# Kernel tuning notes

Hardware: AMD Instinct MI355X
Metric: run time of the kernel (lower is better)

Reference implementation:

```python
import jax, jax.numpy as jnp
import numpy as np

N_NODES = 100000
N_EDGES = 1600000
IN_CH = 128
HID_CH = 128


def setup_inputs() -> dict:
    key = jax.random.key(0)
    ks = jax.random.split(key, 12)
    s = 1.0 / np.sqrt(IN_CH)
    sh = 1.0 / np.sqrt(HID_CH)
    return {
        "x": jax.random.normal(ks[0], (N_NODES, IN_CH), dtype=jnp.float32),
        "edge_index": jax.random.randint(ks[1], (2, N_EDGES), 0, N_NODES, dtype=jnp.int32),
        # SAGEConv1: lin_l (applied to aggregated neighbors, has bias), lin_r (root)
        "W1_l": jax.random.uniform(ks[2], (IN_CH, HID_CH), jnp.float32, -s, s),
        "b1": jax.random.uniform(ks[3], (HID_CH,), jnp.float32, -s, s),
        "W1_r": jax.random.uniform(ks[4], (IN_CH, HID_CH), jnp.float32, -s, s),
        # SAGEConv2
        "W2_l": jax.random.uniform(ks[5], (HID_CH, HID_CH), jnp.float32, -sh, sh),
        "b2": jax.random.uniform(ks[6], (HID_CH,), jnp.float32, -sh, sh),
        "W2_r": jax.random.uniform(ks[7], (HID_CH, HID_CH), jnp.float32, -sh, sh),
        # decoder Linear(hidden, in)
        "Wd": jax.random.uniform(ks[8], (HID_CH, IN_CH), jnp.float32, -sh, sh),
        "bd": jax.random.uniform(ks[9], (IN_CH,), jnp.float32, -sh, sh),
        "alpha": jnp.float32(0.5),
    }


def _sage_conv(h, src, dst, n_nodes, W_l, b, W_r):
    # PyG SAGEConv (mean aggr): out = lin_l(mean_{j in N(i)} x_j) + lin_r(x_i)
    msg = h[src]  # [E, C] gather from source nodes
    agg = jax.ops.segment_sum(msg, dst, num_segments=n_nodes)  # [N, C]
    cnt = jax.ops.segment_sum(jnp.ones((src.shape[0],), h.dtype), dst,
                              num_segments=n_nodes)  # [N]
    mean = agg / jnp.maximum(cnt, 1.0)[:, None]
    return mean @ W_l + b + h @ W_r


def reference(x, edge_index, W1_l, b1, W1_r, W2_l, b2, W2_r, Wd, bd, alpha):
    n_nodes = x.shape[0]
    src, dst = edge_index[0], edge_index[1]
    h = jax.nn.relu(_sage_conv(x, src, dst, n_nodes, W1_l, b1, W1_r))
    # dropout p=0.2 is identity in eval mode
    h = jax.nn.relu(_sage_conv(h, src, dst, n_nodes, W2_l, b2, W2_r))
    x_updated = h @ Wd + bd
    return alpha * x_updated + (1.0 - alpha) * x
```

## Files before the change

### kernel.cpp

```cpp
#include <hip/hip_runtime.h>
#include <cstddef>
#include <cstdint>

#define CH 128
#define NBKT 196
#define ABLK 320
#define BKT_NODES 512

typedef __attribute__((ext_vector_type(8))) short short8;
typedef __attribute__((ext_vector_type(4))) float f32x4;

__device__ __forceinline__ unsigned short f2bf(float f) {
  unsigned u = __float_as_uint(f);
  u += 0x7FFF + ((u >> 16) & 1);
  return (unsigned short)(u >> 16);
}
__device__ __forceinline__ float bf_lo(unsigned int u) {
  return __uint_as_float(u << 16);
}
__device__ __forceinline__ float bf_hi(unsigned int u) {
  return __uint_as_float(u & 0xffff0000u);
}
__device__ __forceinline__ void gld16(const void* g, void* l) {
  __builtin_amdgcn_global_load_lds((const __attribute__((address_space(1))) unsigned int*)g,
                                   (__attribute__((address_space(3))) unsigned int*)l, 16, 0, 0);
}

__global__ void k_cvt(const float4* __restrict__ in, uint4* __restrict__ out, int n8) {
  int i = blockIdx.x * 256 + threadIdx.x;
  if (i < n8) {
    float4 a = in[i * 2], b = in[i * 2 + 1];
    uint4 o;
    o.x = (unsigned)f2bf(a.x) | ((unsigned)f2bf(a.y) << 16);
    o.y = (unsigned)f2bf(a.z) | ((unsigned)f2bf(a.w) << 16);
    o.z = (unsigned)f2bf(b.x) | ((unsigned)f2bf(b.y) << 16);
    o.w = (unsigned)f2bf(b.z) | ((unsigned)f2bf(b.w) << 16);
    out[i] = o;
  }
}

__global__ void k_wt(const float* __restrict__ w0, const float* __restrict__ w1,
                     const float* __restrict__ w2, const float* __restrict__ w3,
                     const float* __restrict__ w4, unsigned short* __restrict__ dst) {
  const float* srcs[5] = {w0, w1, w2, w3, w4};
  const float* w = srcs[blockIdx.x];
  unsigned short* d = dst + (size_t)blockIdx.x * CH * CH;
  for (int idx = threadIdx.x; idx < CH * CH; idx += 256) {
    int k = idx >> 7, nn = idx & 127;
    d[nn * CH + k] = f2bf(w[idx]);
  }
}

__global__ void k_bhist(const int* __restrict__ dst, int* __restrict__ cnt, int E, int chunk) {
  __shared__ int c[NBKT];
  for (int i = threadIdx.x; i < NBKT; i += 256) c[i] = 0;
  __syncthreads();
  int s = blockIdx.x * chunk;
  int e = min(s + chunk, E);
  for (int i = s + threadIdx.x; i < e; i += 256)
    atomicAdd(&c[dst[i] >> 9], 1);
  __syncthreads();
  for (int i = threadIdx.x; i < NBKT; i += 256)
    cnt[i * ABLK + blockIdx.x] = c[i];
}

__global__ void k_bin(const int* __restrict__ src, const int* __restrict__ dst,
                      const int* __restrict__ ofs, unsigned int* __restrict__ binned,
                      int E, int chunk) {
  __shared__ int cur[NBKT];
  for (int i = threadIdx.x; i < NBKT; i += 256) cur[i] = ofs[i * ABLK + blockIdx.x];
  __syncthreads();
  int s = blockIdx.x * chunk;
  int e = min(s + chunk, E);
  for (int i = s + threadIdx.x; i < e; i += 256) {
    int d = dst[i];
    int b = d >> 9;
    int pos = atomicAdd(&cur[b], 1);
    binned[pos] = (unsigned)src[i] | ((unsigned)(d & 511) << 17);
  }
}

__global__ __launch_bounds__(256)
void k_bucket(const unsigned int* __restrict__ binned, const int* __restrict__ ofs,
              int* __restrict__ rowptr, int* __restrict__ sorted, int N, int E, int nbkt) {
  __shared__ int c[BKT_NODES];
  __shared__ int tsum[256];
  __shared__ int cur[BKT_NODES];
  int b = blockIdx.x, t = threadIdx.x;
  int s = ofs[b * ABLK];
  int e = ofs[(b + 1) * ABLK];
  c[t] = 0; c[t + 256] = 0;
  __syncthreads();
  for (int i = s + t; i < e; i += 256)
    atomicAdd(&c[binned[i] >> 17], 1);
  __syncthreads();
  int v0 = c[2 * t], v1 = c[2 * t + 1];
  int tot = v0 + v1;
  tsum[t] = tot;
  __syncthreads();
  for (int o = 1; o < 256; o <<= 1) {
    int y = (t >= o) ? tsum[t - o] : 0;
    __syncthreads();
    tsum[t] += y;
    __syncthreads();
  }
  int excl = tsum[t] - tot;
  int base = b * BKT_NODES;
  int r0 = s + excl, r1 = s + excl + v0;
  if (base + 2 * t < N)     rowptr[base + 2 * t]     = r0;
  if (base + 2 * t + 1 < N) rowptr[base + 2 * t + 1] = r1;
  cur[2 * t] = r0; cur[2 * t + 1] = r1;
  __syncthreads();
  for (int i = s + t; i < e; i += 256) {
    unsigned w = binned[i];
    int pos = atomicAdd(&cur[w >> 17], 1);
    sorted[pos] = w & 0x1FFFF;
  }
  if (b == nbkt - 1 && t == 0) rowptr[N] = E;
}

__global__ void k_scan1(const int* __restrict__ deg, int* __restrict__ rowptr,
                        int* __restrict__ bsums, int n) {
  __shared__ int sh[256];
  int tid = threadIdx.x;
  int base = blockIdx.x * 1024 + tid * 4;
  int v0 = (base + 0 < n) ? deg[base + 0] : 0;
  int v1 = (base + 1 < n) ? deg[base + 1] : 0;
  int v2 = (base + 2 < n) ? deg[base + 2] : 0;
  int v3 = (base + 3 < n) ? deg[base + 3] : 0;
  int tot = v0 + v1 + v2 + v3;
  sh[tid] = tot;
  __syncthreads();
  for (int off = 1; off < 256; off <<= 1) {
    int y = (tid >= off) ? sh[tid - off] : 0;
    __syncthreads();
    sh[tid] += y;
    __syncthreads();
  }
  int excl = sh[tid] - tot;
  if (base + 0 < n) rowptr[base + 0] = excl;
  if (base + 1 < n) rowptr[base + 1] = excl + v0;
  if (base + 2 < n) rowptr[base + 2] = excl + v0 + v1;
  if (base + 3 < n) rowptr[base + 3] = excl + v0 + v1 + v2;
  if (tid == 255) bsums[blockIdx.x] = sh[255];
}

__global__ void k_scan2(int* __restrict__ bsums, int g) {
  __shared__ int sh[1024];
  int tid = threadIdx.x;
  int v = (tid < g) ? bsums[tid] : 0;
  sh[tid] = v;
  __syncthreads();
  for (int off = 1; off < 1024; off <<= 1) {
    int y = (tid >= off) ? sh[tid - off] : 0;
    __syncthreads();
    sh[tid] += y;
    __syncthreads();
  }
  if (tid < g) bsums[tid] = sh[tid] - v;
}

__global__ void k_scan3(int* __restrict__ arr, const int* __restrict__ bsums, int n, int total) {
  int i = blockIdx.x * 256 + threadIdx.x;
  if (i < n) arr[i] += bsums[i >> 10];
  if (i == 0) arr[n] = total;
}

__global__ __launch_bounds__(256)
void k_agg(const uint2* __restrict__ in2, uint2* __restrict__ out2,
           const int* __restrict__ rowptr, const int* __restrict__ sorted_src,
           int n, int nwaves) {
  int wid = (blockIdx.x * 256 + threadIdx.x) >> 6;
  int lane = threadIdx.x & 63;
  int half = lane >> 5;
  int sl = lane & 31;

  for (int node = wid; node < n; node += nwaves) {
    int beg = rowptr[node], end = rowptr[node + 1];
    float a0 = 0.f, a1 = 0.f, a2 = 0.f, a3 = 0.f;
    int e = beg;
    for (; e + 8 <= end; e += 8) {
      uint2 v[4];
#pragma unroll
      for (int j = 0; j < 4; j++)
        v[j] = in2[((unsigned)sorted_src[e + 2 * j + half] << 5) + sl];
#pragma unroll
      for (int j = 0; j < 4; j++) {
        a0 += bf_lo(v[j].x); a1 += bf_hi(v[j].x);
        a2 += bf_lo(v[j].y); a3 += bf_hi(v[j].y);
      }
    }
    if (e < end) {
      uint2 v[4];
#pragma unroll
      for (int j = 0; j < 4; j++) {
        int k = e + 2 * j + half;
        int idx = (k < end) ? k : beg;
        uint2 tv = in2[((unsigned)sorted_src[idx] << 5) + sl];
        if (k >= end) { tv.x = 0u; tv.y = 0u; }
        v[j] = tv;
      }
#pragma unroll
      for (int j = 0; j < 4; j++) {
        a0 += bf_lo(v[j].x); a1 += bf_hi(v[j].x);
        a2 += bf_lo(v[j].y); a3 += bf_hi(v[j].y);
      }
    }
    a0 += __shfl(a0, lane ^ 32);
    a1 += __shfl(a1, lane ^ 32);
    a2 += __shfl(a2, lane ^ 32);
    a3 += __shfl(a3, lane ^ 32);
    int d = end - beg;
    float inv = (d > 0) ? (1.f / (float)d) : 0.f;
    if (half == 0) {
      uint2 o;
      o.x = (unsigned)f2bf(a0 * inv) | ((unsigned)f2bf(a1 * inv) << 16);
      o.y = (unsigned)f2bf(a2 * inv) | ((unsigned)f2bf(a3 * inv) << 16);
      out2[((unsigned)node << 5) + sl] = o;
    }
  }
}

__global__ __launch_bounds__(256, 2)
void k_sage(const unsigned short* __restrict__ Am, const unsigned short* __restrict__ Ax,
            const unsigned short* __restrict__ WTl, const unsigned short* __restrict__ WTr,
            const float* __restrict__ bias, unsigned short* __restrict__ out, int n) {
  __shared__ unsigned short sA[128 * 64];
  __shared__ unsigned short sB[128 * 64];
  int tid = threadIdx.x;
  int lane = tid & 63;
  int w = tid >> 6;
  int row0 = blockIdx.x * 128;
  int col_lo = lane & 15, quad = lane >> 4;

  f32x4 acc[2][8];
#pragma unroll
  for (int mt = 0; mt < 2; mt++)
#pragma unroll
    for (int nt = 0; nt < 8; nt++) acc[mt][nt] = (f32x4){0.f, 0.f, 0.f, 0.f};

  const unsigned short* As[4] = {Am, Am, Ax, Ax};
  const unsigned short* Bs[4] = {WTl, WTl, WTr, WTr};
  const int k0s[4] = {0, 64, 0, 64};

  for (int c = 0; c < 4; c++) {
    const unsigned short* Ap = As[c];
    const unsigned short* Bp = Bs[c];
    int k0 = k0s[c];
#pragma unroll
    for (int it = 0; it < 4; it++) {
      int flat = it * 256 + tid;
      int r = flat >> 3;
      int kof = (flat & 7) * 8;
      int gr = row0 + r;
      if (gr > n - 1) gr = n - 1;
      gld16(Ap + (size_t)gr * CH + k0 + kof, sA + flat * 8);
      gld16(Bp + (size_t)r * CH + k0 + kof, sB + flat * 8);
    }
    __syncthreads();

#pragma unroll
    for (int ks = 0; ks < 2; ks++) {
      short8 a0 = *(const short8*)&sA[(w * 32 + col_lo) * 64 + ks * 32 + quad * 8];
      short8 a1 = *(const short8*)&sA[(w * 32 + 16 + col_lo) * 64 + ks * 32 + quad * 8];
      short8 b[8];
#pragma unroll
      for (int nt = 0; nt < 8; nt++)
        b[nt] = *(const short8*)&sB[(nt * 16 + col_lo) * 64 + ks * 32 + quad * 8];
#pragma unroll
      for (int nt = 0; nt < 8; nt++) {
        acc[0][nt] = __builtin_amdgcn_mfma_f32_16x16x32_bf16(a0, b[nt], acc[0][nt], 0, 0, 0);
        acc[1][nt] = __builtin_amdgcn_mfma_f32_16x16x32_bf16(a1, b[nt], acc[1][nt], 0, 0, 0);
      }
    }
    __syncthreads();
  }

#pragma unroll
  for (int nt = 0; nt < 8; nt++) {
    float bb = bias[nt * 16 + col_lo];
#pragma unroll
    for (int mt = 0; mt < 2; mt++) {
#pragma unroll
      for (int r = 0; r < 4; r++) {
        int rr = row0 + w * 32 + mt * 16 + quad * 4 + r;
        if (rr < n) {
          float v = fmaxf(acc[mt][nt][r] + bb, 0.f);
          out[(size_t)rr * CH + nt * 16 + col_lo] = f2bf(v);
        }
      }
    }
  }
}

__global__ __launch_bounds__(256, 2)
void k_dec(const unsigned short* __restrict__ H, const unsigned short* __restrict__ WTd,
           const float* __restrict__ bd, const float* __restrict__ X,
           const float* __restrict__ alpha_p, float* __restrict__ out, int n) {
  __shared__ unsigned short sA[128 * 64];
  __shared__ unsigned short sB[128 * 64];
  int tid = threadIdx.x;
  int lane = tid & 63;
  int w = tid >> 6;
  int row0 = blockIdx.x * 128;
  int col_lo = lane & 15, quad = lane >> 4;

  f32x4 acc[2][8];
#pragma unroll
  for (int mt = 0; mt < 2; mt++)
#pragma unroll
    for (int nt = 0; nt < 8; nt++) acc[mt][nt] = (f32x4){0.f, 0.f, 0.f, 0.f};

  for (int c = 0; c < 2; c++) {
    int k0 = c * 64;
#pragma unroll
    for (int it = 0; it < 4; it++) {
      int flat = it * 256 + tid;
      int r = flat >> 3;
      int kof = (flat & 7) * 8;
      int gr = row0 + r;
      if (gr > n - 1) gr = n - 1;
      gld16(H + (size_t)gr * CH + k0 + kof, sA + flat * 8);
      gld16(WTd + (size_t)r * CH + k0 + kof, sB + flat * 8);
    }
    __syncthreads();

#pragma unroll
    for (int ks = 0; ks < 2; ks++) {
      short8 a0 = *(const short8*)&sA[(w * 32 + col_lo) * 64 + ks * 32 + quad * 8];
      short8 a1 = *(const short8*)&sA[(w * 32 + 16 + col_lo) * 64 + ks * 32 + quad * 8];
      short8 b[8];
#pragma unroll
      for (int nt = 0; nt < 8; nt++)
        b[nt] = *(const short8*)&sB[(nt * 16 + col_lo) * 64 + ks * 32 + quad * 8];
#pragma unroll
      for (int nt = 0; nt < 8; nt++) {
        acc[0][nt] = __builtin_amdgcn_mfma_f32_16x16x32_bf16(a0, b[nt], acc[0][nt], 0, 0, 0);
        acc[1][nt] = __builtin_amdgcn_mfma_f32_16x16x32_bf16(a1, b[nt], acc[1][nt], 0, 0, 0);
      }
    }
    __syncthreads();
  }

  float al = alpha_p[0];
  float be = 1.f - al;
#pragma unroll
  for (int nt = 0; nt < 8; nt++) {
    float bb = bd[nt * 16 + col_lo];
#pragma unroll
    for (int mt = 0; mt < 2; mt++) {
#pragma unroll
      for (int r = 0; r < 4; r++) {
        int rr = row0 + w * 32 + mt * 16 + quad * 4 + r;
        if (rr < n) {
          int cc = nt * 16 + col_lo;
          float xv = X[(size_t)rr * CH + cc];
          out[(size_t)rr * CH + cc] = al * (acc[mt][nt][r] + bb) + be * xv;
        }
      }
    }
  }
}


extern "C" void kernel_launch(void* const* d_in, const int* in_sizes, int n_in,
                              void* d_out, int out_size, void* d_ws, size_t ws_size,
                              hipStream_t stream) {
  const float* x   = (const float*)d_in[0];
  const int*   ei  = (const int*)d_in[1];
  const float* W1l = (const float*)d_in[2];
  const float* b1  = (const float*)d_in[3];
  const float* W1r = (const float*)d_in[4];
  const float* W2l = (const float*)d_in[5];
  const float* b2  = (const float*)d_in[6];
  const float* W2r = (const float*)d_in[7];
  const float* Wd  = (const float*)d_in[8];
  const float* bd  = (const float*)d_in[9];
  const float* alp = (const float*)d_in[10];

  int N = in_sizes[0] / CH;
  int E = in_sizes[1] / 2;
  const int* src = ei;
  const int* dst = ei + E;

  char* ws = (char*)d_ws;
  size_t off = 0;
  auto alloc = [&](size_t bytes) -> char* {
    off = (off + 511) & ~size_t(511);
    char* p = ws + off;
    off += bytes;
    return p;
  };
  int*   rowptr = (int*)alloc((size_t)(N + 1) * 4);
  int*   ofs    = (int*)alloc((size_t)(NBKT * ABLK + 1) * 4);
  int*   bsums  = (int*)alloc(4096);
  int*   sorted = (int*)alloc((size_t)E * 4);
  unsigned short* xb = (unsigned short*)alloc((size_t)N * CH * 2);
  unsigned short* h  = (unsigned short*)alloc((size_t)N * CH * 2);
  unsigned short* WT = (unsigned short*)alloc((size_t)5 * CH * CH * 2);
  unsigned short* mean = (unsigned short*)d_out;
  unsigned int* binned = (unsigned int*)((char*)d_out + (size_t)N * CH * 2);

  int chunk = (E + ABLK - 1) / ABLK;
  int nA = NBKT * ABLK;
  int GA = (nA + 1023) / 1024;

  k_cvt<<<(N * CH / 8 + 255) / 256, 256, 0, stream>>>((const float4*)x, (uint4*)xb, N * CH / 8);
  k_wt<<<5, 256, 0, stream>>>(W1l, W1r, W2l, W2r, Wd, WT);

  k_bhist<<<ABLK, 256, 0, stream>>>(dst, ofs, E, chunk);
  k_scan1<<<GA, 256, 0, stream>>>(ofs, ofs, bsums, nA);
  k_scan2<<<1, 1024, 0, stream>>>(bsums, GA);
  k_scan3<<<(nA + 255) / 256, 256, 0, stream>>>(ofs, bsums, nA, E);
  k_bin<<<ABLK, 256, 0, stream>>>(src, dst, ofs, binned, E, chunk);
  k_bucket<<<NBKT, 256, 0, stream>>>(binned, ofs, rowptr, sorted, N, E, NBKT);

  int gAggBlocks = 2048;
  int nWaves = gAggBlocks * 4;
  int gGemm = (N + 127) / 128;
  unsigned short* WT1l = WT + 0 * CH * CH;
  unsigned short* WT1r = WT + 1 * CH * CH;
  unsigned short* WT2l = WT + 2 * CH * CH;
  unsigned short* WT2r = WT + 3 * CH * CH;
  unsigned short* WTd  = WT + 4 * CH * CH;

  k_agg<<<gAggBlocks, 256, 0, stream>>>((const uint2*)xb, (uint2*)mean, rowptr, sorted, N, nWaves);
  k_sage<<<gGemm, 256, 0, stream>>>(mean, xb, WT1l, WT1r, b1, h, N);
  k_agg<<<gAggBlocks, 256, 0, stream>>>((const uint2*)h, (uint2*)mean, rowptr, sorted, N, nWaves);
  k_sage<<<gGemm, 256, 0, stream>>>(mean, h, WT2l, WT2r, b2, h, N);
  k_dec<<<gGemm, 256, 0, stream>>>(h, WTd, bd, x, alp, (float*)d_out, N);
}
```

Baseline: 421.3 us.

## Gather neighbor features in FP8 and merge prep and scan kernels

Node features are now also stored as FP8 copies (x at conversion time, h in the first SAGE epilogue), and the aggregation kernel gathers these 1-byte values instead of bf16. This halves the bytes moved by the random-access neighbor gather, which is the dominant memory cost. The weight-transpose, histogram and x-conversion kernels are merged into one launch, and the three-kernel scan is replaced by a single-block scan, cutting launch count. The cost is FP8 quantization error in the mean aggregation, extra stores in the conversion and GEMM epilogue, and a serial single-block scan.

```diff
diff --git a/kernel.cpp b/kernel.cpp
--- a/kernel.cpp
+++ b/kernel.cpp
@@ -9,59 +9,100 @@
 
 typedef __attribute__((ext_vector_type(8))) short short8;
 typedef __attribute__((ext_vector_type(4))) float f32x4;
+typedef __attribute__((ext_vector_type(2))) float f32x2;
 
 __device__ __forceinline__ unsigned short f2bf(float f) {
   unsigned u = __float_as_uint(f);
   u += 0x7FFF + ((u >> 16) & 1);
   return (unsigned short)(u >> 16);
 }
-__device__ __forceinline__ float bf_lo(unsigned int u) {
-  return __uint_as_float(u << 16);
-}
-__device__ __forceinline__ float bf_hi(unsigned int u) {
-  return __uint_as_float(u & 0xffff0000u);
-}
 __device__ __forceinline__ void gld16(const void* g, void* l) {
   __builtin_amdgcn_global_load_lds((const __attribute__((address_space(1))) unsigned int*)g,
                                    (__attribute__((address_space(3))) unsigned int*)l, 16, 0, 0);
 }
-
-__global__ void k_cvt(const float4* __restrict__ in, uint4* __restrict__ out, int n8) {
-  int i = blockIdx.x * 256 + threadIdx.x;
-  if (i < n8) {
-    float4 a = in[i * 2], b = in[i * 2 + 1];
-    uint4 o;
-    o.x = (unsigned)f2bf(a.x) | ((unsigned)f2bf(a.y) << 16);
-    o.y = (unsigned)f2bf(a.z) | ((unsigned)f2bf(a.w) << 16);
-    o.z = (unsigned)f2bf(b.x) | ((unsigned)f2bf(b.y) << 16);
-    o.w = (unsigned)f2bf(b.z) | ((unsigned)f2bf(b.w) << 16);
-    out[i] = o;
-  }
-}
-
-__global__ void k_wt(const float* __restrict__ w0, const float* __restrict__ w1,
-                     const float* __restrict__ w2, const float* __restrict__ w3,
-                     const float* __restrict__ w4, unsigned short* __restrict__ dst) {
-  const float* srcs[5] = {w0, w1, w2, w3, w4};
-  const float* w = srcs[blockIdx.x];
-  unsigned short* d = dst + (size_t)blockIdx.x * CH * CH;
-  for (int idx = threadIdx.x; idx < CH * CH; idx += 256) {
-    int k = idx >> 7, nn = idx & 127;
-    d[nn * CH + k] = f2bf(w[idx]);
-  }
-}
-
-__global__ void k_bhist(const int* __restrict__ dst, int* __restrict__ cnt, int E, int chunk) {
+__device__ __forceinline__ unsigned int pk_fp8x4(float a, float b, float c, float d) {
+  int p = __builtin_amdgcn_cvt_pk_fp8_f32(a, b, 0, false);
+  p = __builtin_amdgcn_cvt_pk_fp8_f32(c, d, p, true);
+  return (unsigned int)p;
+}
+
+__global__ __launch_bounds__(256)
+void k_prep(const float* __restrict__ w0, const float* __restrict__ w1,
+            const float* __restrict__ w2, const float* __restrict__ w3,
+            const float* __restrict__ w4, unsigned short* __restrict__ wt,
+            const int* __restrict__ dst, int* __restrict__ cnt, int E, int chunk,
+            const float4* __restrict__ x4, uint4* __restrict__ xb,
+            uint2* __restrict__ xb8, int n8) {
   __shared__ int c[NBKT];
-  for (int i = threadIdx.x; i < NBKT; i += 256) c[i] = 0;
-  __syncthreads();
-  int s = blockIdx.x * chunk;
-  int e = min(s + chunk, E);
-  for (int i = s + threadIdx.x; i < e; i += 256)
-    atomicAdd(&c[dst[i] >> 9], 1);
-  __syncthreads();
-  for (int i = threadIdx.x; i < NBKT; i += 256)
-    cnt[i * ABLK + blockIdx.x] = c[i];
+  int b = blockIdx.x, t = threadIdx.x;
+  if (b < 5) {
+    const float* srcs[5] = {w0, w1, w2, w3, w4};
+    const float* w = srcs[b];
+    unsigned short* d = wt + (size_t)b * CH * CH;
+    for (int idx = t; idx < CH * CH; idx += 256) {
+      int k = idx >> 7, nn = idx & 127;
+      d[nn * CH + k] = f2bf(w[idx]);
+    }
+  } else if (b < 5 + ABLK) {
+    int ab = b - 5;
+    for (int i = t; i < NBKT; i += 256) c[i] = 0;
+    __syncthreads();
+    int s = ab * chunk;
+    int e = min(s + chunk, E);
+    for (int i = s + t; i < e; i += 256)
+      atomicAdd(&c[dst[i] >> 9], 1);
+    __syncthreads();
+    for (int i = t; i < NBKT; i += 256)
+      cnt[i * ABLK + ab] = c[i];
+  } else {
+    int i = (b - 5 - ABLK) * 256 + t;
+    if (i < n8) {
+      float4 a = x4[i * 2], bb = x4[i * 2 + 1];
+      uint4 o;
+      o.x = (unsigned)f2bf(a.x) | ((unsigned)f2bf(a.y) << 16);
+      o.y = (unsigned)f2bf(a.z) | ((unsigned)f2bf(a.w) << 16);
+      o.z = (unsigned)f2bf(bb.x) | ((unsigned)f2bf(bb.y) << 16);
+      o.w = (unsigned)f2bf(bb.z) | ((unsigned)f2bf(bb.w) << 16);
+      xb[i] = o;
+      uint2 o8;
+      o8.x = pk_fp8x4(a.x, a.y, a.z, a.w);
+      o8.y = pk_fp8x4(bb.x, bb.y, bb.z, bb.w);
+      xb8[i] = o8;
+    }
+  }
+}
+
+__global__ __launch_bounds__(1024)
+void k_scanA(int* __restrict__ arr, int n, int total) {
+  __shared__ int sh[1024];
+  int t = threadIdx.x;
+  int run = 0;
+  int tiles = (n + 4095) >> 12;
+  for (int tt = 0; tt < tiles; tt++) {
+    int base = (tt << 12) + t * 4;
+    int v0 = (base + 0 < n) ? arr[base + 0] : 0;
+    int v1 = (base + 1 < n) ? arr[base + 1] : 0;
+    int v2 = (base + 2 < n) ? arr[base + 2] : 0;
+    int v3 = (base + 3 < n) ? arr[base + 3] : 0;
+    int tot = v0 + v1 + v2 + v3;
+    sh[t] = tot;
+    __syncthreads();
+    for (int o = 1; o < 1024; o <<= 1) {
+      int y = (t >= o) ? sh[t - o] : 0;
+      __syncthreads();
+      sh[t] += y;
+      __syncthreads();
+    }
+    int excl = sh[t] - tot + run;
+    int tile_total = sh[1023];
+    if (base + 0 < n) arr[base + 0] = excl;
+    if (base + 1 < n) arr[base + 1] = excl + v0;
+    if (base + 2 < n) arr[base + 2] = excl + v0 + v1;
+    if (base + 3 < n) arr[base + 3] = excl + v0 + v1 + v2;
+    run += tile_total;
+    __syncthreads();
+  }
+  if (t == 0) arr[n] = total;
 }
 
 __global__ void k_bin(const int* __restrict__ src, const int* __restrict__ dst,
@@ -119,57 +160,10 @@
   if (b == nbkt - 1 && t == 0) rowptr[N] = E;
 }
 
-__global__ void k_scan1(const int* __restrict__ deg, int* __restrict__ rowptr,
-                        int* __restrict__ bsums, int n) {
-  __shared__ int sh[256];
-  int tid = threadIdx.x;
-  int base = blockIdx.x * 1024 + tid * 4;
-  int v0 = (base + 0 < n) ? deg[base + 0] : 0;
-  int v1 = (base + 1 < n) ? deg[base + 1] : 0;
-  int v2 = (base + 2 < n) ? deg[base + 2] : 0;
-  int v3 = (base + 3 < n) ? deg[base + 3] : 0;
-  int tot = v0 + v1 + v2 + v3;
-  sh[tid] = tot;
-  __syncthreads();
-  for (int off = 1; off < 256; off <<= 1) {
-    int y = (tid >= off) ? sh[tid - off] : 0;
-    __syncthreads();
-    sh[tid] += y;
-    __syncthreads();
-  }
-  int excl = sh[tid] - tot;
-  if (base + 0 < n) rowptr[base + 0] = excl;
-  if (base + 1 < n) rowptr[base + 1] = excl + v0;
-  if (base + 2 < n) rowptr[base + 2] = excl + v0 + v1;
-  if (base + 3 < n) rowptr[base + 3] = excl + v0 + v1 + v2;
-  if (tid == 255) bsums[blockIdx.x] = sh[255];
-}
-
-__global__ void k_scan2(int* __restrict__ bsums, int g) {
-  __shared__ int sh[1024];
-  int tid = threadIdx.x;
-  int v = (tid < g) ? bsums[tid] : 0;
-  sh[tid] = v;
-  __syncthreads();
-  for (int off = 1; off < 1024; off <<= 1) {
-    int y = (tid >= off) ? sh[tid - off] : 0;
-    __syncthreads();
-    sh[tid] += y;
-    __syncthreads();
-  }
-  if (tid < g) bsums[tid] = sh[tid] - v;
-}
-
-__global__ void k_scan3(int* __restrict__ arr, const int* __restrict__ bsums, int n, int total) {
-  int i = blockIdx.x * 256 + threadIdx.x;
-  if (i < n) arr[i] += bsums[i >> 10];
-  if (i == 0) arr[n] = total;
-}
-
 __global__ __launch_bounds__(256)
-void k_agg(const uint2* __restrict__ in2, uint2* __restrict__ out2,
-           const int* __restrict__ rowptr, const int* __restrict__ sorted_src,
-           int n, int nwaves) {
+void k_agg8(const unsigned int* __restrict__ in8, uint2* __restrict__ outb,
+            const int* __restrict__ rowptr, const int* __restrict__ sorted_src,
+            int n, int nwaves) {
   int wid = (blockIdx.x * 256 + threadIdx.x) >> 6;
   int lane = threadIdx.x & 63;
   int half = lane >> 5;
@@ -180,30 +174,31 @@
     float a0 = 0.f, a1 = 0.f, a2 = 0.f, a3 = 0.f;
     int e = beg;
     for (; e + 8 <= end; e += 8) {
-      uint2 v[4];
+      unsigned int v[4];
 #pragma unroll
       for (int j = 0; j < 4; j++)
-        v[j] = in2[((unsigned)sorted_src[e + 2 * j + half] << 5) + sl];
+        v[j] = in8[((unsigned)sorted_src[e + 2 * j + half] << 5) + sl];
 #pragma unroll
       for (int j = 0; j < 4; j++) {
-        a0 += bf_lo(v[j].x); a1 += bf_hi(v[j].x);
-        a2 += bf_lo(v[j].y); a3 += bf_hi(v[j].y);
+        f32x2 lo = __builtin_amdgcn_cvt_pk_f32_fp8(v[j], false);
+        f32x2 hi = __builtin_amdgcn_cvt_pk_f32_fp8(v[j], true);
+        a0 += lo.x; a1 += lo.y; a2 += hi.x; a3 += hi.y;
       }
     }
     if (e < end) {
-      uint2 v[4];
+      unsigned int v[4];
 #pragma unroll
       for (int j = 0; j < 4; j++) {
         int k = e + 2 * j + half;
         int idx = (k < end) ? k : beg;
-        uint2 tv = in2[((unsigned)sorted_src[idx] << 5) + sl];
-        if (k >= end) { tv.x = 0u; tv.y = 0u; }
-        v[j] = tv;
+        unsigned int tv = in8[((unsigned)sorted_src[idx] << 5) + sl];
+        v[j] = (k < end) ? tv : 0u;
       }
 #pragma unroll
       for (int j = 0; j < 4; j++) {
-        a0 += bf_lo(v[j].x); a1 += bf_hi(v[j].x);
-        a2 += bf_lo(v[j].y); a3 += bf_hi(v[j].y);
+        f32x2 lo = __builtin_amdgcn_cvt_pk_f32_fp8(v[j], false);
+        f32x2 hi = __builtin_amdgcn_cvt_pk_f32_fp8(v[j], true);
+        a0 += lo.x; a1 += lo.y; a2 += hi.x; a3 += hi.y;
       }
     }
     a0 += __shfl(a0, lane ^ 32);
@@ -216,7 +211,7 @@
       uint2 o;
       o.x = (unsigned)f2bf(a0 * inv) | ((unsigned)f2bf(a1 * inv) << 16);
       o.y = (unsigned)f2bf(a2 * inv) | ((unsigned)f2bf(a3 * inv) << 16);
-      out2[((unsigned)node << 5) + sl] = o;
+      outb[((unsigned)node << 5) + sl] = o;
     }
   }
 }
@@ -224,7 +219,8 @@
 __global__ __launch_bounds__(256, 2)
 void k_sage(const unsigned short* __restrict__ Am, const unsigned short* __restrict__ Ax,
             const unsigned short* __restrict__ WTl, const unsigned short* __restrict__ WTr,
-            const float* __restrict__ bias, unsigned short* __restrict__ out, int n) {
+            const float* __restrict__ bias, unsigned short* __restrict__ out,
+            unsigned char* __restrict__ out8, int n) {
   __shared__ unsigned short sA[128 * 64];
   __shared__ unsigned short sB[128 * 64];
   int tid = threadIdx.x;
@@ -285,8 +281,13 @@
       for (int r = 0; r < 4; r++) {
         int rr = row0 + w * 32 + mt * 16 + quad * 4 + r;
         if (rr < n) {
+          int cc = nt * 16 + col_lo;
           float v = fmaxf(acc[mt][nt][r] + bb, 0.f);
-          out[(size_t)rr * CH + nt * 16 + col_lo] = f2bf(v);
+          out[(size_t)rr * CH + cc] = f2bf(v);
+          if (out8) {
+            int p = __builtin_amdgcn_cvt_pk_fp8_f32(v, v, 0, false);
+            out8[(size_t)rr * CH + cc] = (unsigned char)(p & 0xff);
+          }
         }
       }
     }
@@ -393,25 +394,27 @@
   };
   int*   rowptr = (int*)alloc((size_t)(N + 1) * 4);
   int*   ofs    = (int*)alloc((size_t)(NBKT * ABLK + 1) * 4);
-  int*   bsums  = (int*)alloc(4096);
   int*   sorted = (int*)alloc((size_t)E * 4);
   unsigned short* xb = (unsigned short*)alloc((size_t)N * CH * 2);
   unsigned short* h  = (unsigned short*)alloc((size_t)N * CH * 2);
   unsigned short* WT = (unsigned short*)alloc((size_t)5 * CH * CH * 2);
-  unsigned short* mean = (unsigned short*)d_out;
-  unsigned int* binned = (unsigned int*)((char*)d_out + (size_t)N * CH * 2);
+
+  unsigned short* mean  = (unsigned short*)d_out;
+  unsigned char* xb8    = (unsigned char*)d_out + (size_t)N * CH * 2;
+  char*          upper  = (char*)d_out + (size_t)N * CH * 3;
+  unsigned int* binned  = (unsigned int*)upper;
+  unsigned char* h8     = (unsigned char*)upper;
 
   int chunk = (E + ABLK - 1) / ABLK;
   int nA = NBKT * ABLK;
-  int GA = (nA + 1023) / 1024;
-
-  k_cvt<<<(N * CH / 8 + 255) / 256, 256, 0, stream>>>((const float4*)x, (uint4*)xb, N * CH / 8);
-  k_wt<<<5, 256, 0, stream>>>(W1l, W1r, W2l, W2r, Wd, WT);
-
-  k_bhist<<<ABLK, 256, 0, stream>>>(dst, ofs, E, chunk);
-  k_scan1<<<GA, 256, 0, stream>>>(ofs, ofs, bsums, nA);
-  k_scan2<<<1, 1024, 0, stream>>>(bsums, GA);
-  k_scan3<<<(nA + 255) / 256, 256, 0, stream>>>(ofs, bsums, nA, E);
+  int n8 = N * CH / 8;
+  int gCvt = (n8 + 255) / 256;
+
+  k_prep<<<5 + ABLK + gCvt, 256, 0, stream>>>(W1l, W1r, W2l, W2r, Wd, WT,
+                                              dst, ofs, E, chunk,
+                                              (const float4*)x, (uint4*)xb,
+                                              (uint2*)xb8, n8);
+  k_scanA<<<1, 1024, 0, stream>>>(ofs, nA, E);
   k_bin<<<ABLK, 256, 0, stream>>>(src, dst, ofs, binned, E, chunk);
   k_bucket<<<NBKT, 256, 0, stream>>>(binned, ofs, rowptr, sorted, N, E, NBKT);
 
@@ -424,9 +427,11 @@
   unsigned short* WT2r = WT + 3 * CH * CH;
   unsigned short* WTd  = WT + 4 * CH * CH;
 
-  k_agg<<<gAggBlocks, 256, 0, stream>>>((const uint2*)xb, (uint2*)mean, rowptr, sorted, N, nWaves);
-  k_sage<<<gGemm, 256, 0, stream>>>(mean, xb, WT1l, WT1r, b1, h, N);
-  k_agg<<<gAggBlocks, 256, 0, stream>>>((const uint2*)h, (uint2*)mean, rowptr, sorted, N, nWaves);
-  k_sage<<<gGemm, 256, 0, stream>>>(mean, h, WT2l, WT2r, b2, h, N);
+  k_agg8<<<gAggBlocks, 256, 0, stream>>>((const unsigned int*)xb8, (uint2*)mean,
+                                         rowptr, sorted, N, nWaves);
+  k_sage<<<gGemm, 256, 0, stream>>>(mean, xb, WT1l, WT1r, b1, h, h8, N);
+  k_agg8<<<gAggBlocks, 256, 0, stream>>>((const unsigned int*)h8, (uint2*)mean,
+                                         rowptr, sorted, N, nWaves);
+  k_sage<<<gGemm, 256, 0, stream>>>(mean, h, WT2l, WT2r, b2, h, (unsigned char*)nullptr, N);
   k_dec<<<gGemm, 256, 0, stream>>>(h, WTd, bd, x, alp, (float*)d_out, N);
 }
```

Result: slower. 433.3 us (+2.9%).
